# Kernel optimization log

Hardware: AMD Instinct MI355X
Metric: run time of the kernel (lower is better)

The kernel has to match this reference:

```python
import jax, jax.numpy as jnp
import numpy as np

H = 1024
NH = 16
HD = H // NH  # 64

def setup_inputs() -> dict:
    key = jax.random.key(0)
    ks = jax.random.split(key, 6)
    B, S = 2, 2048
    hidden_states = jax.random.normal(ks[0], (B, S, H), dtype=jnp.float32)
    attention_mask = jnp.ones((B, S), dtype=jnp.int32)
    sc = 1.0 / np.sqrt(H)
    Wq = jax.random.normal(ks[1], (H, H), dtype=jnp.float32) * sc
    Wk = jax.random.normal(ks[2], (H, H), dtype=jnp.float32) * sc
    Wv = jax.random.normal(ks[3], (H, H), dtype=jnp.float32) * sc
    Wo = jax.random.normal(ks[4], (H, H), dtype=jnp.float32) * sc
    return {"hidden_states": hidden_states, "attention_mask": attention_mask,
            "Wq": Wq, "Wk": Wk, "Wv": Wv, "Wo": Wo}

def reference(hidden_states, attention_mask, Wq, Wk, Wv, Wo):
    B, S, _ = hidden_states.shape
    # nn.Linear(bias=False): y = x @ W.T
    q = hidden_states @ Wq.T
    k = hidden_states @ Wk.T
    v = hidden_states @ Wv.T
    # [B, NH, S, HD]
    q = q.reshape(B, S, NH, HD).transpose(0, 2, 1, 3)
    k = k.reshape(B, S, NH, HD).transpose(0, 2, 1, 3)
    v = v.reshape(B, S, NH, HD).transpose(0, 2, 1, 3)
    # ELU+1 feature map
    q = jax.nn.elu(q) + 1.0
    k = jax.nn.elu(k) + 1.0
    # [B, NH, S, S]
    attn = jnp.einsum('bhqd,bhkd->bhqk', q, k)
    mask = attention_mask[:, None, None, :]  # [B,1,1,S]
    attn = jnp.where(mask == 0, -jnp.inf, attn)
    attn = jax.nn.softmax(attn, axis=-1)
    # dropout p=0.0 (eval) -> identity
    out = jnp.einsum('bhqk,bhkd->bhqd', attn, v)
    out = out.transpose(0, 2, 1, 3).reshape(B, S, H)
    return out @ Wo.T
```

## Files before the change

### kernel.cpp

```cpp
#include <hip/hip_runtime.h>

#define H_ 1024
#define NH_ 16
#define HD_ 64
#define B_ 2
#define S_ 2048
#define BS_ 4096

typedef _Float16 half8 __attribute__((ext_vector_type(8)));
typedef _Float16 half4_t __attribute__((ext_vector_type(4)));
typedef float floatx4 __attribute__((ext_vector_type(4)));

#define LOG2E 1.44269504088896f

__device__ __forceinline__ void async_copy16(void* lds, const void* g) {
  __builtin_amdgcn_global_load_lds(
      (const __attribute__((address_space(1))) unsigned int*)g,
      (__attribute__((address_space(3))) unsigned int*)lds, 16, 0, 0);
}

__device__ __forceinline__ half8 cvt8(float4 lo, float4 hi) {
  half8 h;
  h[0] = (_Float16)lo.x; h[1] = (_Float16)lo.y;
  h[2] = (_Float16)lo.z; h[3] = (_Float16)lo.w;
  h[4] = (_Float16)hi.x; h[5] = (_Float16)hi.y;
  h[6] = (_Float16)hi.z; h[7] = (_Float16)hi.w;
  return h;
}

__global__ __launch_bounds__(256, 3) void qkv_gemm(
    const float* __restrict__ A, const float* __restrict__ Wq,
    const float* __restrict__ Wk, const float* __restrict__ Wv,
    _Float16* __restrict__ qh, _Float16* __restrict__ kh,
    _Float16* __restrict__ vt) {
  const int d = blockIdx.x;
  const int y = d & 31;
  const int k = d >> 5;
  const int x = k & 7;
  const int z = k >> 3;
  const float* W = (z == 0) ? Wq : (z == 1) ? Wk : Wv;
  const int rbase = y * 128;
  const int cbase = x * 128;
  __shared__ _Float16 SM[16896];
  const int tid = threadIdx.x, lane = tid & 63, w = tid >> 6;
  const int quad = lane >> 4, l16 = lane & 15;
  const int wr = (w >> 1) * 64, wc = (w & 1) * 64;

  floatx4 zero = {0.f, 0.f, 0.f, 0.f};
  floatx4 acc[4][4];
#pragma unroll
  for (int i = 0; i < 4; ++i)
#pragma unroll
    for (int j = 0; j < 4; ++j) acc[i][j] = zero;

  const int srow = tid >> 2;
  const int pslot = tid & 3;
  const int sslot = pslot ^ ((srow >> 1) & 3);
  const float* Ag = A + (size_t)(rbase + srow) * H_ + sslot * 8;
  const float* Bg = W + (size_t)(cbase + srow) * H_ + sslot * 8;

  float4 ra[4], rb[4];
  auto LOAD = [&](int t) {
    const int k0 = t * 32;
    ra[0] = *(const float4*)(Ag + k0);
    ra[1] = *(const float4*)(Ag + k0 + 4);
    ra[2] = *(const float4*)(Ag + (size_t)64 * H_ + k0);
    ra[3] = *(const float4*)(Ag + (size_t)64 * H_ + k0 + 4);
    rb[0] = *(const float4*)(Bg + k0);
    rb[1] = *(const float4*)(Bg + k0 + 4);
    rb[2] = *(const float4*)(Bg + (size_t)64 * H_ + k0);
    rb[3] = *(const float4*)(Bg + (size_t)64 * H_ + k0 + 4);
  };
  auto WRITE = [&](int s) {
    _Float16* ab = &SM[s * 4096 + tid * 8];
    _Float16* bb = &SM[8192 + s * 4096 + tid * 8];
    *(half8*)ab = cvt8(ra[0], ra[1]);
    *(half8*)(ab + 2048) = cvt8(ra[2], ra[3]);
    *(half8*)bb = cvt8(rb[0], rb[1]);
    *(half8*)(bb + 2048) = cvt8(rb[2], rb[3]);
  };

  const int rsw = (l16 >> 1) & 3;
  auto COMPUTE = [&](int s) {
    const _Float16* Ap = &SM[s * 4096];
    const _Float16* Bp = &SM[8192 + s * 4096];
    half8 af[4], bf[4];
#pragma unroll
    for (int t = 0; t < 4; ++t)
      af[t] = *(const half8*)&Ap[(wr + t * 16 + l16) * 32 + (quad ^ rsw) * 8];
#pragma unroll
    for (int t = 0; t < 4; ++t)
      bf[t] = *(const half8*)&Bp[(wc + t * 16 + l16) * 32 + (quad ^ rsw) * 8];
    __builtin_amdgcn_s_setprio(1);
#pragma unroll
    for (int i = 0; i < 4; ++i)
#pragma unroll
      for (int j = 0; j < 4; ++j)
        acc[i][j] = __builtin_amdgcn_mfma_f32_16x16x32_f16(af[i], bf[j],
                                                           acc[i][j], 0, 0, 0);
    __builtin_amdgcn_s_setprio(0);
  };

  LOAD(0);
  for (int t = 0; t < 32; ++t) {
    __syncthreads();
    WRITE(t & 1);
    if (t < 31) LOAD(t + 1);
    asm volatile("s_waitcnt lgkmcnt(0)" ::: "memory");
    __builtin_amdgcn_s_barrier();
    __builtin_amdgcn_sched_barrier(0);
    COMPUTE(t & 1);
  }

  __syncthreads();
  const int PAD = 132;
  const int b = rbase >> 11, sl_base = rbase & (S_ - 1);
  if (z != 2) {
    const float scale = (z == 0) ? LOG2E : 1.0f;
#pragma unroll
    for (int i = 0; i < 4; ++i) {
      int s0 = wr + i * 16 + quad * 4;
#pragma unroll
      for (int j = 0; j < 4; ++j) {
        int c = wc + j * 16 + l16;
#pragma unroll
        for (int r = 0; r < 4; ++r) {
          float xx = acc[i][j][r];
          xx = ((xx > 0.f) ? (xx + 1.f) : __expf(xx)) * scale;
          SM[(s0 + r) * PAD + c] = (_Float16)xx;
        }
      }
    }
    __syncthreads();
    _Float16* outp = (z == 0) ? qh : kh;
#pragma unroll
    for (int k2 = 0; k2 < 8; ++k2) {
      int c2 = tid + k2 * 256;
      int s = c2 >> 4, part = c2 & 15;
      int col = cbase + part * 8;
      int h = col >> 6, dd = col & 63;
      half8 vvv = *(const half8*)&SM[s * PAD + part * 8];
      *(half8*)&outp[((size_t)(b * NH_ + h) * S_ + sl_base + s) * HD_ + dd] = vvv;
    }
  } else {
#pragma unroll
    for (int i = 0; i < 4; ++i) {
      int s0 = wr + i * 16 + quad * 4;
#pragma unroll
      for (int j = 0; j < 4; ++j) {
        int c = wc + j * 16 + l16;
#pragma unroll
        for (int r = 0; r < 4; ++r)
          SM[c * PAD + s0 + r] = (_Float16)acc[i][j][r];
      }
    }
    __syncthreads();
#pragma unroll
    for (int k2 = 0; k2 < 8; ++k2) {
      int c2 = tid + k2 * 256;
      int c = c2 >> 4, part = c2 & 15;
      int col = cbase + c;
      int h = col >> 6, dd = col & 63;
      half8 vvv = *(const half8*)&SM[c * PAD + part * 8];
      *(half8*)&vt[((size_t)(b * NH_ + h) * HD_ + dd) * S_ + sl_base + part * 8] = vvv;
    }
  }
}

__global__ __launch_bounds__(256, 2) void flash_attn(
    const _Float16* __restrict__ qh, const _Float16* __restrict__ kh,
    const _Float16* __restrict__ vt, const int* __restrict__ mask,
    _Float16* __restrict__ attn_out) {
  const int dd = blockIdx.x;
  const int bh = dd & 31, b = bh >> 4, h = bh & 15;
  const int qbase = (dd >> 5) * 128;
  const int tid = threadIdx.x, w = tid >> 6, lane = tid & 63;
  const int quad = lane >> 4, l16 = lane & 15;

  __shared__ _Float16 Kt[2][128 * 64];
  __shared__ _Float16 Vt[2][64 * 128];

  const _Float16* Q = qh + (size_t)bh * (S_ * HD_);
  const _Float16* K = kh + (size_t)bh * (S_ * HD_);
  const _Float16* Vg = vt + (size_t)bh * (HD_ * S_);
  const int* Mb = mask + b * S_;

  half8 qf[2][2];
#pragma unroll
  for (int g = 0; g < 2; ++g) {
    int qr = qbase + w * 32 + g * 16 + l16;
    qf[g][0] = *(const half8*)&Q[qr * 64 + quad * 8];
    qf[g][1] = *(const half8*)&Q[qr * 64 + 32 + quad * 8];
  }

  floatx4 zero = {0.f, 0.f, 0.f, 0.f};
  floatx4 o[2][4];
#pragma unroll
  for (int g = 0; g < 2; ++g)
#pragma unroll
    for (int i = 0; i < 4; ++i) o[g][i] = zero;
  float mi[2] = {-3e38f, -3e38f}, li[2] = {0.f, 0.f};

  const int krow_off = lane >> 3;
  const int kslot = lane & 7;
  const int kchunk = kslot ^ (krow_off & 7);
  const int vrow_off = lane >> 4;
  const int vslot = lane & 15;

  {
#pragma unroll
    for (int u = 0; u < 4; ++u) {
      int kl = w * 32 + u * 8;
      async_copy16(&Kt[0][kl * 64], K + (size_t)(kl + krow_off) * 64 + kchunk * 8);
    }
#pragma unroll
    for (int u = 0; u < 4; ++u) {
      int d0 = w * 16 + u * 4 + vrow_off;
      int c0 = vslot ^ (d0 & 15);
      async_copy16(&Vt[0][(w * 16 + u * 4) * 128], Vg + (size_t)d0 * S_ + c0 * 8);
    }
  }

  for (int kt = 0; kt < S_ / 128; ++kt) {
    const int key0 = kt * 128;
    const int buf = kt & 1;
    __syncthreads();
    if (kt < S_ / 128 - 1) {
      const int key1 = key0 + 128;
#pragma unroll
      for (int u = 0; u < 4; ++u) {
        int kl = w * 32 + u * 8;
        async_copy16(&Kt[buf ^ 1][kl * 64],
                     K + (size_t)(key1 + kl + krow_off) * 64 + kchunk * 8);
      }
#pragma unroll
      for (int u = 0; u < 4; ++u) {
        int d0 = w * 16 + u * 4 + vrow_off;
        int c0 = vslot ^ (d0 & 15);
        async_copy16(&Vt[buf ^ 1][(w * 16 + u * 4) * 128],
                     Vg + (size_t)d0 * S_ + key1 + c0 * 8);
      }
    }
    int m0 = Mb[key0 + lane];
    int m1 = Mb[key0 + 64 + lane];

    const _Float16* Kb = &Kt[buf][0];
    const _Float16* Vb = &Vt[buf][0];

    floatx4 sa[2][8];
#pragma unroll
    for (int g = 0; g < 2; ++g)
#pragma unroll
      for (int ct = 0; ct < 8; ++ct) sa[g][ct] = zero;
    {
      int s0 = quad ^ (l16 & 7);
      int s1 = (4 + quad) ^ (l16 & 7);
#pragma unroll
      for (int ct = 0; ct < 8; ++ct) {
        int key = ct * 16 + l16;
        half8 bf0 = *(half8*)&Kb[key * 64 + s0 * 8];
        half8 bf1 = *(half8*)&Kb[key * 64 + s1 * 8];
        sa[0][ct] = __builtin_amdgcn_mfma_f32_16x16x32_f16(bf0, qf[0][0], sa[0][ct], 0, 0, 0);
        sa[0][ct] = __builtin_amdgcn_mfma_f32_16x16x32_f16(bf1, qf[0][1], sa[0][ct], 0, 0, 0);
        sa[1][ct] = __builtin_amdgcn_mfma_f32_16x16x32_f16(bf0, qf[1][0], sa[1][ct], 0, 0, 0);
        sa[1][ct] = __builtin_amdgcn_mfma_f32_16x16x32_f16(bf1, qf[1][1], sa[1][ct], 0, 0, 0);
      }
    }
    if (__any((m0 == 0) || (m1 == 0))) {
#pragma unroll
      for (int ct = 0; ct < 8; ++ct)
#pragma unroll
        for (int r = 0; r < 4; ++r)
          if (Mb[key0 + ct * 16 + quad * 4 + r] == 0) {
            sa[0][ct][r] = -1e30f;
            sa[1][ct][r] = -1e30f;
          }
    }
#pragma unroll
    for (int g = 0; g < 2; ++g) {
      float mx = sa[g][0][0];
#pragma unroll
      for (int ct = 0; ct < 8; ++ct)
#pragma unroll
        for (int r = 0; r < 4; ++r) mx = fmaxf(mx, sa[g][ct][r]);
      mx = fmaxf(mx, __shfl_xor(mx, 16));
      mx = fmaxf(mx, __shfl_xor(mx, 32));
      float mn = fmaxf(mi[g], mx);
      float alpha = __builtin_amdgcn_exp2f(mi[g] - mn);
      mi[g] = mn;
      float rs = 0.f;
#pragma unroll
      for (int ct = 0; ct < 8; ++ct)
#pragma unroll
        for (int r = 0; r < 4; ++r) {
          float p = __builtin_amdgcn_exp2f(sa[g][ct][r] - mn);
          sa[g][ct][r] = p;
          rs += p;
        }
      rs += __shfl_xor(rs, 16);
      rs += __shfl_xor(rs, 32);
      li[g] = li[g] * alpha + rs;
#pragma unroll
      for (int ct2 = 0; ct2 < 4; ++ct2) {
        o[g][ct2][0] *= alpha; o[g][ct2][1] *= alpha;
        o[g][ct2][2] *= alpha; o[g][ct2][3] *= alpha;
      }
    }
#pragma unroll
    for (int ct = 0; ct < 8; ++ct) {
      half4_t p0, p1;
#pragma unroll
      for (int r = 0; r < 4; ++r) {
        p0[r] = (_Float16)sa[0][ct][r];
        p1[r] = (_Float16)sa[1][ct][r];
      }
      int chunk = (2 * ct + (quad >> 1)) ^ l16;
      int off = chunk * 8 + (quad & 1) * 4;
#pragma unroll
      for (int ct2 = 0; ct2 < 4; ++ct2) {
        int dx = ct2 * 16 + l16;
        half4_t vf = *(half4_t*)&Vb[dx * 128 + off];
        o[0][ct2] = __builtin_amdgcn_mfma_f32_16x16x16f16(vf, p0, o[0][ct2], 0, 0, 0);
        o[1][ct2] = __builtin_amdgcn_mfma_f32_16x16x16f16(vf, p1, o[1][ct2], 0, 0, 0);
      }
    }
  }
#pragma unroll
  for (int g = 0; g < 2; ++g) {
    float inv = 1.0f / li[g];
    int row = qbase + w * 32 + g * 16 + l16;
#pragma unroll
    for (int ct2 = 0; ct2 < 4; ++ct2) {
      half4_t pk;
#pragma unroll
      for (int r = 0; r < 4; ++r) pk[r] = (_Float16)(o[g][ct2][r] * inv);
      int dx = ct2 * 16 + quad * 4;
      *(half4_t*)&attn_out[((size_t)(b * S_ + row)) * H_ + h * HD_ + dx] = pk;
    }
  }
}

__global__ __launch_bounds__(256, 2) void out_gemm(
    const _Float16* __restrict__ A, const float* __restrict__ W,
    float* __restrict__ out) {
  const int d = blockIdx.x;
  const int y = d & 31;
  const int x = d >> 5;
  const int rbase = y * 128;
  const int cbase = x * 64;
  __shared__ _Float16 SM[24576];
  const int tid = threadIdx.x, lane = tid & 63, w = tid >> 6;
  const int quad = lane >> 4, l16 = lane & 15;

  floatx4 zero = {0.f, 0.f, 0.f, 0.f};
  floatx4 acc[2][4];
#pragma unroll
  for (int i = 0; i < 2; ++i)
#pragma unroll
    for (int j = 0; j < 4; ++j) acc[i][j] = zero;

  const int srow = tid >> 3;
  const int pslot = tid & 7;
  const int sslot = pslot ^ (srow & 7);
  const _Float16* Ag = A + (size_t)(rbase + srow) * H_ + sslot * 8;
  const float* Bg = W + (size_t)(cbase + srow) * H_ + sslot * 8;

  half8 qa[4];
  float4 rb[4];
  auto LOAD = [&](int t) {
    const int k0 = t * 64;
#pragma unroll
    for (int u = 0; u < 4; ++u)
      qa[u] = *(const half8*)(Ag + (size_t)(u * 32) * H_ + k0);
    rb[0] = *(const float4*)(Bg + k0);
    rb[1] = *(const float4*)(Bg + k0 + 4);
    rb[2] = *(const float4*)(Bg + (size_t)32 * H_ + k0);
    rb[3] = *(const float4*)(Bg + (size_t)32 * H_ + k0 + 4);
  };
  auto WRITE = [&](int s) {
    _Float16* ab = &SM[s * 8192 + tid * 8];
    _Float16* bb = &SM[16384 + s * 4096 + tid * 8];
#pragma unroll
    for (int u = 0; u < 4; ++u) *(half8*)(ab + u * 2048) = qa[u];
    *(half8*)bb = cvt8(rb[0], rb[1]);
    *(half8*)(bb + 2048) = cvt8(rb[2], rb[3]);
  };

  const int rsw = l16 & 7;
  auto COMPUTE = [&](int s) {
    const _Float16* Ap = &SM[s * 8192];
    const _Float16* Bp = &SM[16384 + s * 4096];
    half8 af[2][2], bf[4][2];
#pragma unroll
    for (int i = 0; i < 2; ++i)
#pragma unroll
      for (int hh = 0; hh < 2; ++hh)
        af[i][hh] = *(const half8*)&Ap[(w * 32 + i * 16 + l16) * 64 +
                                       (((hh * 4 + quad) ^ rsw) * 8)];
#pragma unroll
    for (int j = 0; j < 4; ++j)
#pragma unroll
      for (int hh = 0; hh < 2; ++hh)
        bf[j][hh] = *(const half8*)&Bp[(j * 16 + l16) * 64 +
                                       (((hh * 4 + quad) ^ rsw) * 8)];
    __builtin_amdgcn_s_setprio(1);
#pragma unroll
    for (int i = 0; i < 2; ++i)
#pragma unroll
      for (int j = 0; j < 4; ++j) {
        acc[i][j] = __builtin_amdgcn_mfma_f32_16x16x32_f16(af[i][0], bf[j][0],
                                                           acc[i][j], 0, 0, 0);
        acc[i][j] = __builtin_amdgcn_mfma_f32_16x16x32_f16(af[i][1], bf[j][1],
                                                           acc[i][j], 0, 0, 0);
      }
    __builtin_amdgcn_s_setprio(0);
  };

  LOAD(0);
  for (int t = 0; t < 16; ++t) {
    __syncthreads();
    WRITE(t & 1);
    if (t < 15) LOAD(t + 1);
    asm volatile("s_waitcnt lgkmcnt(0)" ::: "memory");
    __builtin_amdgcn_s_barrier();
    __builtin_amdgcn_sched_barrier(0);
    COMPUTE(t & 1);
  }

  __syncthreads();
  float* FB = (float*)SM;
  const int FPAD = 68;
#pragma unroll
  for (int i = 0; i < 2; ++i) {
    int s0 = w * 32 + i * 16 + quad * 4;
#pragma unroll
    for (int j = 0; j < 4; ++j) {
      int c = j * 16 + l16;
#pragma unroll
      for (int r = 0; r < 4; ++r)
        FB[(s0 + r) * FPAD + c] = acc[i][j][r];
    }
  }
  __syncthreads();
#pragma unroll
  for (int k2 = 0; k2 < 8; ++k2) {
    int c2 = tid + k2 * 256;
    int s = c2 >> 4, part = c2 & 15;
    *(float4*)&out[(size_t)(rbase + s) * H_ + cbase + part * 4] =
        *(float4*)&FB[s * FPAD + part * 4];
  }
}

extern "C" void kernel_launch(void* const* d_in, const int* in_sizes, int n_in,
                              void* d_out, int out_size, void* d_ws,
                              size_t ws_size, hipStream_t stream) {
  const float* hs = (const float*)d_in[0];
  const int* mask = (const int*)d_in[1];
  const float* Wq = (const float*)d_in[2];
  const float* Wk = (const float*)d_in[3];
  const float* Wv = (const float*)d_in[4];
  const float* Wo = (const float*)d_in[5];
  float* out = (float*)d_out;

  _Float16* p = (_Float16*)d_ws;
  _Float16* q_h = p;  p += (size_t)BS_ * H_;
  _Float16* k_h = p;  p += (size_t)BS_ * H_;
  _Float16* v_t = p;  p += (size_t)BS_ * H_;
  _Float16* ao_h = p; p += (size_t)BS_ * H_;

  qkv_gemm<<<768, 256, 0, stream>>>(hs, Wq, Wk, Wv, q_h, k_h, v_t);
  flash_attn<<<512, 256, 0, stream>>>(q_h, k_h, v_t, mask, ao_h);
  out_gemm<<<512, 256, 0, stream>>>(ao_h, Wo, out);
}
```

Baseline: 189.7 us.

## Fuse flash attention and output projection via grid-wide atomic barrier

Merges the attention kernel and the output GEMM into one persistent launch of 512 blocks. A global atomic counter acts as a grid barrier, so every block finishes its attention tile before any block starts its slice of the output projection. This removes one kernel launch and the gap between the two kernels. In exchange it adds a memset and a spin-wait, and it deadlocks unless all 512 blocks are resident at the same time, which relies on two blocks per CU fitting given the 64KB of shared memory each block uses.

```diff
diff --git a/kernel.cpp b/kernel.cpp
--- a/kernel.cpp
+++ b/kernel.cpp
@@ -167,287 +167,299 @@
   }
 }
 
-__global__ __launch_bounds__(256, 2) void flash_attn(
+__global__ __launch_bounds__(256, 2) void attn_out_fused(
     const _Float16* __restrict__ qh, const _Float16* __restrict__ kh,
     const _Float16* __restrict__ vt, const int* __restrict__ mask,
-    _Float16* __restrict__ attn_out) {
-  const int dd = blockIdx.x;
-  const int bh = dd & 31, b = bh >> 4, h = bh & 15;
-  const int qbase = (dd >> 5) * 128;
+    _Float16* ao, const float* __restrict__ Wo, float* __restrict__ out,
+    unsigned int* ctr) {
+  __shared__ _Float16 SMEM[32768];
+  const int blk = blockIdx.x;
   const int tid = threadIdx.x, w = tid >> 6, lane = tid & 63;
   const int quad = lane >> 4, l16 = lane & 15;
 
-  __shared__ _Float16 Kt[2][128 * 64];
-  __shared__ _Float16 Vt[2][64 * 128];
-
-  const _Float16* Q = qh + (size_t)bh * (S_ * HD_);
-  const _Float16* K = kh + (size_t)bh * (S_ * HD_);
-  const _Float16* Vg = vt + (size_t)bh * (HD_ * S_);
-  const int* Mb = mask + b * S_;
-
-  half8 qf[2][2];
-#pragma unroll
-  for (int g = 0; g < 2; ++g) {
-    int qr = qbase + w * 32 + g * 16 + l16;
-    qf[g][0] = *(const half8*)&Q[qr * 64 + quad * 8];
-    qf[g][1] = *(const half8*)&Q[qr * 64 + 32 + quad * 8];
-  }
-
-  floatx4 zero = {0.f, 0.f, 0.f, 0.f};
-  floatx4 o[2][4];
-#pragma unroll
-  for (int g = 0; g < 2; ++g)
-#pragma unroll
-    for (int i = 0; i < 4; ++i) o[g][i] = zero;
-  float mi[2] = {-3e38f, -3e38f}, li[2] = {0.f, 0.f};
-
-  const int krow_off = lane >> 3;
-  const int kslot = lane & 7;
-  const int kchunk = kslot ^ (krow_off & 7);
-  const int vrow_off = lane >> 4;
-  const int vslot = lane & 15;
-
   {
-#pragma unroll
-    for (int u = 0; u < 4; ++u) {
-      int kl = w * 32 + u * 8;
-      async_copy16(&Kt[0][kl * 64], K + (size_t)(kl + krow_off) * 64 + kchunk * 8);
-    }
-#pragma unroll
-    for (int u = 0; u < 4; ++u) {
-      int d0 = w * 16 + u * 4 + vrow_off;
-      int c0 = vslot ^ (d0 & 15);
-      async_copy16(&Vt[0][(w * 16 + u * 4) * 128], Vg + (size_t)d0 * S_ + c0 * 8);
-    }
-  }
-
-  for (int kt = 0; kt < S_ / 128; ++kt) {
-    const int key0 = kt * 128;
-    const int buf = kt & 1;
-    __syncthreads();
-    if (kt < S_ / 128 - 1) {
-      const int key1 = key0 + 128;
+    const int bh = blk & 31, b = bh >> 4, h = bh & 15;
+    const int qbase = (blk >> 5) * 128;
+    _Float16* Kt0 = &SMEM[0];
+    _Float16* Vt0 = &SMEM[16384];
+
+    const _Float16* Q = qh + (size_t)bh * (S_ * HD_);
+    const _Float16* K = kh + (size_t)bh * (S_ * HD_);
+    const _Float16* Vg = vt + (size_t)bh * (HD_ * S_);
+    const int* Mb = mask + b * S_;
+
+    half8 qf[2][2];
+#pragma unroll
+    for (int g = 0; g < 2; ++g) {
+      int qr = qbase + w * 32 + g * 16 + l16;
+      qf[g][0] = *(const half8*)&Q[qr * 64 + quad * 8];
+      qf[g][1] = *(const half8*)&Q[qr * 64 + 32 + quad * 8];
+    }
+
+    floatx4 zero = {0.f, 0.f, 0.f, 0.f};
+    floatx4 o[2][4];
+#pragma unroll
+    for (int g = 0; g < 2; ++g)
+#pragma unroll
+      for (int i = 0; i < 4; ++i) o[g][i] = zero;
+    float mi[2] = {-3e38f, -3e38f}, li[2] = {0.f, 0.f};
+
+    const int krow_off = lane >> 3;
+    const int kslot = lane & 7;
+    const int kchunk = kslot ^ (krow_off & 7);
+    const int vrow_off = lane >> 4;
+    const int vslot = lane & 15;
+
+    {
 #pragma unroll
       for (int u = 0; u < 4; ++u) {
         int kl = w * 32 + u * 8;
-        async_copy16(&Kt[buf ^ 1][kl * 64],
-                     K + (size_t)(key1 + kl + krow_off) * 64 + kchunk * 8);
+        async_copy16(Kt0 + kl * 64, K + (size_t)(kl + krow_off) * 64 + kchunk * 8);
       }
 #pragma unroll
       for (int u = 0; u < 4; ++u) {
         int d0 = w * 16 + u * 4 + vrow_off;
         int c0 = vslot ^ (d0 & 15);
-        async_copy16(&Vt[buf ^ 1][(w * 16 + u * 4) * 128],
-                     Vg + (size_t)d0 * S_ + key1 + c0 * 8);
-      }
-    }
-    int m0 = Mb[key0 + lane];
-    int m1 = Mb[key0 + 64 + lane];
-
-    const _Float16* Kb = &Kt[buf][0];
-    const _Float16* Vb = &Vt[buf][0];
-
-    floatx4 sa[2][8];
-#pragma unroll
-    for (int g = 0; g < 2; ++g)
-#pragma unroll
-      for (int ct = 0; ct < 8; ++ct) sa[g][ct] = zero;
-    {
-      int s0 = quad ^ (l16 & 7);
-      int s1 = (4 + quad) ^ (l16 & 7);
+        async_copy16(Vt0 + (w * 16 + u * 4) * 128, Vg + (size_t)d0 * S_ + c0 * 8);
+      }
+    }
+
+    for (int kt = 0; kt < S_ / 128; ++kt) {
+      const int key0 = kt * 128;
+      const int buf = kt & 1;
+      __syncthreads();
+      if (kt < S_ / 128 - 1) {
+        const int key1 = key0 + 128;
+        _Float16* Kd = Kt0 + (buf ^ 1) * 8192;
+        _Float16* Vd = Vt0 + (buf ^ 1) * 8192;
+#pragma unroll
+        for (int u = 0; u < 4; ++u) {
+          int kl = w * 32 + u * 8;
+          async_copy16(Kd + kl * 64,
+                       K + (size_t)(key1 + kl + krow_off) * 64 + kchunk * 8);
+        }
+#pragma unroll
+        for (int u = 0; u < 4; ++u) {
+          int d0 = w * 16 + u * 4 + vrow_off;
+          int c0 = vslot ^ (d0 & 15);
+          async_copy16(Vd + (w * 16 + u * 4) * 128,
+                       Vg + (size_t)d0 * S_ + key1 + c0 * 8);
+        }
+      }
+      int m0 = Mb[key0 + lane];
+      int m1 = Mb[key0 + 64 + lane];
+
+      const _Float16* Kb = Kt0 + buf * 8192;
+      const _Float16* Vb = Vt0 + buf * 8192;
+
+      floatx4 sa[2][8];
+#pragma unroll
+      for (int g = 0; g < 2; ++g)
+#pragma unroll
+        for (int ct = 0; ct < 8; ++ct) sa[g][ct] = zero;
+      {
+        int s0 = quad ^ (l16 & 7);
+        int s1 = (4 + quad) ^ (l16 & 7);
+#pragma unroll
+        for (int ct = 0; ct < 8; ++ct) {
+          int key = ct * 16 + l16;
+          half8 bf0 = *(half8*)&Kb[key * 64 + s0 * 8];
+          half8 bf1 = *(half8*)&Kb[key * 64 + s1 * 8];
+          sa[0][ct] = __builtin_amdgcn_mfma_f32_16x16x32_f16(bf0, qf[0][0], sa[0][ct], 0, 0, 0);
+          sa[0][ct] = __builtin_amdgcn_mfma_f32_16x16x32_f16(bf1, qf[0][1], sa[0][ct], 0, 0, 0);
+          sa[1][ct] = __builtin_amdgcn_mfma_f32_16x16x32_f16(bf0, qf[1][0], sa[1][ct], 0, 0, 0);
+          sa[1][ct] = __builtin_amdgcn_mfma_f32_16x16x32_f16(bf1, qf[1][1], sa[1][ct], 0, 0, 0);
+        }
+      }
+      if (__any((m0 == 0) || (m1 == 0))) {
+#pragma unroll
+        for (int ct = 0; ct < 8; ++ct)
+#pragma unroll
+          for (int r = 0; r < 4; ++r)
+            if (Mb[key0 + ct * 16 + quad * 4 + r] == 0) {
+              sa[0][ct][r] = -1e30f;
+              sa[1][ct][r] = -1e30f;
+            }
+      }
+#pragma unroll
+      for (int g = 0; g < 2; ++g) {
+        float mx = sa[g][0][0];
+#pragma unroll
+        for (int ct = 0; ct < 8; ++ct)
+#pragma unroll
+          for (int r = 0; r < 4; ++r) mx = fmaxf(mx, sa[g][ct][r]);
+        mx = fmaxf(mx, __shfl_xor(mx, 16));
+        mx = fmaxf(mx, __shfl_xor(mx, 32));
+        float mn = fmaxf(mi[g], mx);
+        float alpha = __builtin_amdgcn_exp2f(mi[g] - mn);
+        mi[g] = mn;
+        float rs = 0.f;
+#pragma unroll
+        for (int ct = 0; ct < 8; ++ct)
+#pragma unroll
+          for (int r = 0; r < 4; ++r) {
+            float p = __builtin_amdgcn_exp2f(sa[g][ct][r] - mn);
+            sa[g][ct][r] = p;
+            rs += p;
+          }
+        rs += __shfl_xor(rs, 16);
+        rs += __shfl_xor(rs, 32);
+        li[g] = li[g] * alpha + rs;
+#pragma unroll
+        for (int ct2 = 0; ct2 < 4; ++ct2) {
+          o[g][ct2][0] *= alpha; o[g][ct2][1] *= alpha;
+          o[g][ct2][2] *= alpha; o[g][ct2][3] *= alpha;
+        }
+      }
 #pragma unroll
       for (int ct = 0; ct < 8; ++ct) {
-        int key = ct * 16 + l16;
-        half8 bf0 = *(half8*)&Kb[key * 64 + s0 * 8];
-        half8 bf1 = *(half8*)&Kb[key * 64 + s1 * 8];
-        sa[0][ct] = __builtin_amdgcn_mfma_f32_16x16x32_f16(bf0, qf[0][0], sa[0][ct], 0, 0, 0);
-        sa[0][ct] = __builtin_amdgcn_mfma_f32_16x16x32_f16(bf1, qf[0][1], sa[0][ct], 0, 0, 0);
-        sa[1][ct] = __builtin_amdgcn_mfma_f32_16x16x32_f16(bf0, qf[1][0], sa[1][ct], 0, 0, 0);
-        sa[1][ct] = __builtin_amdgcn_mfma_f32_16x16x32_f16(bf1, qf[1][1], sa[1][ct], 0, 0, 0);
-      }
-    }
-    if (__any((m0 == 0) || (m1 == 0))) {
-#pragma unroll
-      for (int ct = 0; ct < 8; ++ct)
-#pragma unroll
-        for (int r = 0; r < 4; ++r)
-          if (Mb[key0 + ct * 16 + quad * 4 + r] == 0) {
-            sa[0][ct][r] = -1e30f;
-            sa[1][ct][r] = -1e30f;
-          }
+        half4_t p0, p1;
+#pragma unroll
+        for (int r = 0; r < 4; ++r) {
+          p0[r] = (_Float16)sa[0][ct][r];
+          p1[r] = (_Float16)sa[1][ct][r];
+        }
+        int chunk = (2 * ct + (quad >> 1)) ^ l16;
+        int off = chunk * 8 + (quad & 1) * 4;
+#pragma unroll
+        for (int ct2 = 0; ct2 < 4; ++ct2) {
+          int dx = ct2 * 16 + l16;
+          half4_t vf = *(half4_t*)&Vb[dx * 128 + off];
+          o[0][ct2] = __builtin_amdgcn_mfma_f32_16x16x16f16(vf, p0, o[0][ct2], 0, 0, 0);
+          o[1][ct2] = __builtin_amdgcn_mfma_f32_16x16x16f16(vf, p1, o[1][ct2], 0, 0, 0);
+        }
+      }
     }
 #pragma unroll
     for (int g = 0; g < 2; ++g) {
-      float mx = sa[g][0][0];
-#pragma unroll
-      for (int ct = 0; ct < 8; ++ct)
-#pragma unroll
-        for (int r = 0; r < 4; ++r) mx = fmaxf(mx, sa[g][ct][r]);
-      mx = fmaxf(mx, __shfl_xor(mx, 16));
-      mx = fmaxf(mx, __shfl_xor(mx, 32));
-      float mn = fmaxf(mi[g], mx);
-      float alpha = __builtin_amdgcn_exp2f(mi[g] - mn);
-      mi[g] = mn;
-      float rs = 0.f;
-#pragma unroll
-      for (int ct = 0; ct < 8; ++ct)
-#pragma unroll
-        for (int r = 0; r < 4; ++r) {
-          float p = __builtin_amdgcn_exp2f(sa[g][ct][r] - mn);
-          sa[g][ct][r] = p;
-          rs += p;
-        }
-      rs += __shfl_xor(rs, 16);
-      rs += __shfl_xor(rs, 32);
-      li[g] = li[g] * alpha + rs;
+      float inv = 1.0f / li[g];
+      int row = qbase + w * 32 + g * 16 + l16;
 #pragma unroll
       for (int ct2 = 0; ct2 < 4; ++ct2) {
-        o[g][ct2][0] *= alpha; o[g][ct2][1] *= alpha;
-        o[g][ct2][2] *= alpha; o[g][ct2][3] *= alpha;
-      }
-    }
-#pragma unroll
-    for (int ct = 0; ct < 8; ++ct) {
-      half4_t p0, p1;
-#pragma unroll
-      for (int r = 0; r < 4; ++r) {
-        p0[r] = (_Float16)sa[0][ct][r];
-        p1[r] = (_Float16)sa[1][ct][r];
-      }
-      int chunk = (2 * ct + (quad >> 1)) ^ l16;
-      int off = chunk * 8 + (quad & 1) * 4;
-#pragma unroll
-      for (int ct2 = 0; ct2 < 4; ++ct2) {
-        int dx = ct2 * 16 + l16;
-        half4_t vf = *(half4_t*)&Vb[dx * 128 + off];
-        o[0][ct2] = __builtin_amdgcn_mfma_f32_16x16x16f16(vf, p0, o[0][ct2], 0, 0, 0);
-        o[1][ct2] = __builtin_amdgcn_mfma_f32_16x16x16f16(vf, p1, o[1][ct2], 0, 0, 0);
+        half4_t pk;
+#pragma unroll
+        for (int r = 0; r < 4; ++r) pk[r] = (_Float16)(o[g][ct2][r] * inv);
+        int dx = ct2 * 16 + quad * 4;
+        *(half4_t*)&ao[((size_t)(b * S_ + row)) * H_ + h * HD_ + dx] = pk;
       }
     }
   }
-#pragma unroll
-  for (int g = 0; g < 2; ++g) {
-    float inv = 1.0f / li[g];
-    int row = qbase + w * 32 + g * 16 + l16;
-#pragma unroll
-    for (int ct2 = 0; ct2 < 4; ++ct2) {
-      half4_t pk;
-#pragma unroll
-      for (int r = 0; r < 4; ++r) pk[r] = (_Float16)(o[g][ct2][r] * inv);
-      int dx = ct2 * 16 + quad * 4;
-      *(half4_t*)&attn_out[((size_t)(b * S_ + row)) * H_ + h * HD_ + dx] = pk;
-    }
-  }
-}
-
-__global__ __launch_bounds__(256, 2) void out_gemm(
-    const _Float16* __restrict__ A, const float* __restrict__ W,
-    float* __restrict__ out) {
-  const int d = blockIdx.x;
-  const int y = d & 31;
-  const int x = d >> 5;
-  const int rbase = y * 128;
-  const int cbase = x * 64;
-  __shared__ _Float16 SM[24576];
-  const int tid = threadIdx.x, lane = tid & 63, w = tid >> 6;
-  const int quad = lane >> 4, l16 = lane & 15;
-
-  floatx4 zero = {0.f, 0.f, 0.f, 0.f};
-  floatx4 acc[2][4];
-#pragma unroll
-  for (int i = 0; i < 2; ++i)
-#pragma unroll
-    for (int j = 0; j < 4; ++j) acc[i][j] = zero;
-
-  const int srow = tid >> 3;
-  const int pslot = tid & 7;
-  const int sslot = pslot ^ (srow & 7);
-  const _Float16* Ag = A + (size_t)(rbase + srow) * H_ + sslot * 8;
-  const float* Bg = W + (size_t)(cbase + srow) * H_ + sslot * 8;
-
-  half8 qa[4];
-  float4 rb[4];
-  auto LOAD = [&](int t) {
-    const int k0 = t * 64;
-#pragma unroll
-    for (int u = 0; u < 4; ++u)
-      qa[u] = *(const half8*)(Ag + (size_t)(u * 32) * H_ + k0);
-    rb[0] = *(const float4*)(Bg + k0);
-    rb[1] = *(const float4*)(Bg + k0 + 4);
-    rb[2] = *(const float4*)(Bg + (size_t)32 * H_ + k0);
-    rb[3] = *(const float4*)(Bg + (size_t)32 * H_ + k0 + 4);
-  };
-  auto WRITE = [&](int s) {
-    _Float16* ab = &SM[s * 8192 + tid * 8];
-    _Float16* bb = &SM[16384 + s * 4096 + tid * 8];
-#pragma unroll
-    for (int u = 0; u < 4; ++u) *(half8*)(ab + u * 2048) = qa[u];
-    *(half8*)bb = cvt8(rb[0], rb[1]);
-    *(half8*)(bb + 2048) = cvt8(rb[2], rb[3]);
-  };
-
-  const int rsw = l16 & 7;
-  auto COMPUTE = [&](int s) {
-    const _Float16* Ap = &SM[s * 8192];
-    const _Float16* Bp = &SM[16384 + s * 4096];
-    half8 af[2][2], bf[4][2];
-#pragma unroll
-    for (int i = 0; i < 2; ++i)
-#pragma unroll
-      for (int hh = 0; hh < 2; ++hh)
-        af[i][hh] = *(const half8*)&Ap[(w * 32 + i * 16 + l16) * 64 +
-                                       (((hh * 4 + quad) ^ rsw) * 8)];
-#pragma unroll
-    for (int j = 0; j < 4; ++j)
-#pragma unroll
-      for (int hh = 0; hh < 2; ++hh)
-        bf[j][hh] = *(const half8*)&Bp[(j * 16 + l16) * 64 +
-                                       (((hh * 4 + quad) ^ rsw) * 8)];
-    __builtin_amdgcn_s_setprio(1);
-#pragma unroll
-    for (int i = 0; i < 2; ++i)
-#pragma unroll
-      for (int j = 0; j < 4; ++j) {
-        acc[i][j] = __builtin_amdgcn_mfma_f32_16x16x32_f16(af[i][0], bf[j][0],
-                                                           acc[i][j], 0, 0, 0);
-        acc[i][j] = __builtin_amdgcn_mfma_f32_16x16x32_f16(af[i][1], bf[j][1],
-                                                           acc[i][j], 0, 0, 0);
-      }
-    __builtin_amdgcn_s_setprio(0);
-  };
-
-  LOAD(0);
-  for (int t = 0; t < 16; ++t) {
-    __syncthreads();
-    WRITE(t & 1);
-    if (t < 15) LOAD(t + 1);
-    asm volatile("s_waitcnt lgkmcnt(0)" ::: "memory");
-    __builtin_amdgcn_s_barrier();
-    __builtin_amdgcn_sched_barrier(0);
-    COMPUTE(t & 1);
-  }
 
   __syncthreads();
-  float* FB = (float*)SM;
-  const int FPAD = 68;
-#pragma unroll
-  for (int i = 0; i < 2; ++i) {
-    int s0 = w * 32 + i * 16 + quad * 4;
-#pragma unroll
-    for (int j = 0; j < 4; ++j) {
-      int c = j * 16 + l16;
-#pragma unroll
-      for (int r = 0; r < 4; ++r)
-        FB[(s0 + r) * FPAD + c] = acc[i][j][r];
-    }
+  if (tid == 0) {
+    __threadfence();
+    atomicAdd(ctr, 1u);
+    while (__hip_atomic_load(ctr, __ATOMIC_ACQUIRE,
+                             __HIP_MEMORY_SCOPE_AGENT) < 512u)
+      __builtin_amdgcn_s_sleep(2);
+    __threadfence();
   }
   __syncthreads();
-#pragma unroll
-  for (int k2 = 0; k2 < 8; ++k2) {
-    int c2 = tid + k2 * 256;
-    int s = c2 >> 4, part = c2 & 15;
-    *(float4*)&out[(size_t)(rbase + s) * H_ + cbase + part * 4] =
-        *(float4*)&FB[s * FPAD + part * 4];
+
+  {
+    const int y = blk & 31;
+    const int x = blk >> 5;
+    const int rbase = y * 128;
+    const int cbase = x * 64;
+    _Float16* SM = SMEM;
+
+    floatx4 zero = {0.f, 0.f, 0.f, 0.f};
+    floatx4 acc[2][4];
+#pragma unroll
+    for (int i = 0; i < 2; ++i)
+#pragma unroll
+      for (int j = 0; j < 4; ++j) acc[i][j] = zero;
+
+    const int srow = tid >> 3;
+    const int pslot = tid & 7;
+    const int sslot = pslot ^ (srow & 7);
+    const _Float16* Ag = ao + (size_t)(rbase + srow) * H_ + sslot * 8;
+    const float* Bg = Wo + (size_t)(cbase + srow) * H_ + sslot * 8;
+
+    half8 qa[4];
+    float4 rb[4];
+    auto LOAD = [&](int t) {
+      const int k0 = t * 64;
+#pragma unroll
+      for (int u = 0; u < 4; ++u)
+        qa[u] = *(const half8*)(Ag + (size_t)(u * 32) * H_ + k0);
+      rb[0] = *(const float4*)(Bg + k0);
+      rb[1] = *(const float4*)(Bg + k0 + 4);
+      rb[2] = *(const float4*)(Bg + (size_t)32 * H_ + k0);
+      rb[3] = *(const float4*)(Bg + (size_t)32 * H_ + k0 + 4);
+    };
+    auto WRITE = [&](int s) {
+      _Float16* ab = &SM[s * 8192 + tid * 8];
+      _Float16* bb = &SM[16384 + s * 4096 + tid * 8];
+#pragma unroll
+      for (int u = 0; u < 4; ++u) *(half8*)(ab + u * 2048) = qa[u];
+      *(half8*)bb = cvt8(rb[0], rb[1]);
+      *(half8*)(bb + 2048) = cvt8(rb[2], rb[3]);
+    };
+
+    const int rsw = l16 & 7;
+    auto COMPUTE = [&](int s) {
+      const _Float16* Ap = &SM[s * 8192];
+      const _Float16* Bp = &SM[16384 + s * 4096];
+      half8 af[2][2], bf[4][2];
+#pragma unroll
+      for (int i = 0; i < 2; ++i)
+#pragma unroll
+        for (int hh = 0; hh < 2; ++hh)
+          af[i][hh] = *(const half8*)&Ap[(w * 32 + i * 16 + l16) * 64 +
+                                         (((hh * 4 + quad) ^ rsw) * 8)];
+#pragma unroll
+      for (int j = 0; j < 4; ++j)
+#pragma unroll
+        for (int hh = 0; hh < 2; ++hh)
+          bf[j][hh] = *(const half8*)&Bp[(j * 16 + l16) * 64 +
+                                         (((hh * 4 + quad) ^ rsw) * 8)];
+      __builtin_amdgcn_s_setprio(1);
+#pragma unroll
+      for (int i = 0; i < 2; ++i)
+#pragma unroll
+        for (int j = 0; j < 4; ++j) {
+          acc[i][j] = __builtin_amdgcn_mfma_f32_16x16x32_f16(af[i][0], bf[j][0],
+                                                             acc[i][j], 0, 0, 0);
+          acc[i][j] = __builtin_amdgcn_mfma_f32_16x16x32_f16(af[i][1], bf[j][1],
+                                                             acc[i][j], 0, 0, 0);
+        }
+      __builtin_amdgcn_s_setprio(0);
+    };
+
+    LOAD(0);
+    for (int t = 0; t < 16; ++t) {
+      __syncthreads();
+      WRITE(t & 1);
+      if (t < 15) LOAD(t + 1);
+      asm volatile("s_waitcnt lgkmcnt(0)" ::: "memory");
+      __builtin_amdgcn_s_barrier();
+      __builtin_amdgcn_sched_barrier(0);
+      COMPUTE(t & 1);
+    }
+
+    __syncthreads();
+    float* FB = (float*)SMEM;
+    const int FPAD = 68;
+#pragma unroll
+    for (int i = 0; i < 2; ++i) {
+      int s0 = w * 32 + i * 16 + quad * 4;
+#pragma unroll
+      for (int j = 0; j < 4; ++j) {
+        int c = j * 16 + l16;
+#pragma unroll
+        for (int r = 0; r < 4; ++r)
+          FB[(s0 + r) * FPAD + c] = acc[i][j][r];
+      }
+    }
+    __syncthreads();
+#pragma unroll
+    for (int k2 = 0; k2 < 8; ++k2) {
+      int c2 = tid + k2 * 256;
+      int s = c2 >> 4, part = c2 & 15;
+      *(float4*)&out[(size_t)(rbase + s) * H_ + cbase + part * 4] =
+          *(float4*)&FB[s * FPAD + part * 4];
+    }
   }
 }
 
@@ -467,8 +479,10 @@
   _Float16* k_h = p;  p += (size_t)BS_ * H_;
   _Float16* v_t = p;  p += (size_t)BS_ * H_;
   _Float16* ao_h = p; p += (size_t)BS_ * H_;
-
+  unsigned int* ctr = (unsigned int*)p;
+
+  hipMemsetAsync(ctr, 0, 4, stream);
   qkv_gemm<<<768, 256, 0, stream>>>(hs, Wq, Wk, Wv, q_h, k_h, v_t);
-  flash_attn<<<512, 256, 0, stream>>>(q_h, k_h, v_t, mask, ao_h);
-  out_gemm<<<512, 256, 0, stream>>>(ao_h, Wo, out);
+  attn_out_fused<<<512, 256, 0, stream>>>(q_h, k_h, v_t, mask, ao_h, Wo, out,
+                                          ctr);
 }
```

New measurement: 274.2 us. 1.45x slower.
